# Optimization experiments

Hardware: AMD Instinct MI355X
Metric: run time of the kernel (lower is better)

The kernel has to match this reference:

```python
import jax, jax.numpy as jnp
import numpy as np

BETA = 0.25
N_EMBED = 1024
DIM = 256


def setup_inputs() -> dict:
    key = jax.random.key(0)
    k1, k2 = jax.random.split(key)
    z = jax.random.normal(k1, (8, DIM, 64, 64), dtype=jnp.float32)
    # matches nn.Embedding init: uniform(-1/n_embed, 1/n_embed)
    codebook = jax.random.uniform(
        k2, (N_EMBED, DIM), dtype=jnp.float32,
        minval=-1.0 / N_EMBED, maxval=1.0 / N_EMBED)
    return {"z": z, "codebook": codebook}


def reference(z, codebook):
    B, C, H, W = z.shape
    sg = jax.lax.stop_gradient
    zp = jnp.transpose(z, (0, 2, 3, 1))          # [B,H,W,C]
    zf = zp.reshape(-1, C)                        # [N,C], N = B*H*W
    # squared euclidean distances: ||z||^2 + ||e||^2 - 2 z.e
    d = (jnp.sum(zf * zf, axis=1, keepdims=True)
         + jnp.sum(codebook * codebook, axis=1)
         - 2.0 * zf @ codebook.T)                 # [N, n_embed]
    idx = jnp.argmin(d, axis=1)                   # [N]
    # one-hot @ codebook in the original is just an index gather
    z_q = codebook[idx].reshape(zp.shape)         # [B,H,W,C]
    loss = (BETA * jnp.mean((sg(z_q) - zp) ** 2)
            + jnp.mean((z_q - sg(zp)) ** 2))
    z_q_st = zp + sg(z_q - zp)                    # straight-through estimator
    z_q_out = jnp.transpose(z_q_st, (0, 3, 1, 2))  # back to NCHW
    return z_q_out, loss, idx.reshape(B, H, W)
```

## Files before the change

kernel.cpp:

```cpp
#include <hip/hip_runtime.h>
#include <hip/hip_fp16.h>

#define NELEM 8388608
#define M_GAP 6e-4f
#define SCORE_SCALE (-1.0f / 512.0f)

typedef _Float16 f16x8 __attribute__((ext_vector_type(8)));
typedef short s16x8 __attribute__((ext_vector_type(8)));
typedef float f32x4 __attribute__((ext_vector_type(4)));

__device__ __forceinline__ unsigned short bf16r(float f) {
  unsigned u = __float_as_uint(f);
  return (unsigned short)((u + 0x7fffu + ((u >> 16) & 1u)) >> 16);
}
__device__ __forceinline__ float bf16f(unsigned short h) {
  return __uint_as_float(((unsigned)h) << 16);
}

__device__ __forceinline__ float pw128_sq(const float* p, int s) {
  float r[8];
#pragma unroll
  for (int j = 0; j < 8; ++j) { float v = p[j * s]; r[j] = __fmul_rn(v, v); }
#pragma unroll
  for (int i = 8; i < 128; i += 8) {
#pragma unroll
    for (int j = 0; j < 8; ++j) {
      float v = p[(i + j) * s];
      r[j] = __fadd_rn(r[j], __fmul_rn(v, v));
    }
  }
  return __fadd_rn(__fadd_rn(__fadd_rn(r[0], r[1]), __fadd_rn(r[2], r[3])),
                   __fadd_rn(__fadd_rn(r[4], r[5]), __fadd_rn(r[6], r[7])));
}
__device__ __forceinline__ float np_sumsq256(const float* p, int s) {
  return __fadd_rn(pw128_sq(p, s), pw128_sq(p + 128 * s, s));
}

__global__ __launch_bounds__(256)
void vq_prep(const float* __restrict__ cb, unsigned short* __restrict__ cbimg,
             float* __restrict__ cbT, float* __restrict__ Bsg,
             unsigned* __restrict__ cnt, float* __restrict__ loss) {
  int gid = blockIdx.x * 256 + threadIdx.x;
  if (gid == 0) { *cnt = 0u; *loss = 0.0f; }
  int j = gid >> 2, qt = gid & 3;
  const float4* row4 = reinterpret_cast<const float4*>(cb + (size_t)j * 256 + qt * 64);
  int T = j >> 4, jj = j & 15;
  unsigned short* baseh = cbimg + (size_t)T * 4096 + jj * 256;
  int sw = jj << 3;
#pragma unroll
  for (int m = 0; m < 8; ++m) {
    int c0 = qt * 64 + m * 8;
    float4 va = row4[m * 2];
    float4 vb = row4[m * 2 + 1];
    float v[8] = {va.x, va.y, va.z, va.w, vb.x, vb.y, vb.z, vb.w};
    s16x8 hv;
#pragma unroll
    for (int q = 0; q < 8; ++q) {
      hv[q] = (short)__half_as_ushort(__float2half(v[q] * 1024.0f));
      cbT[(size_t)(c0 + q) * 1024 + j] = v[q];
    }
    *reinterpret_cast<s16x8*>(baseh + (c0 ^ sw)) = hv;
  }
  if (qt == 0) Bsg[j] = np_sumsq256(cb + (size_t)j * 256, 1);
}

__global__ __launch_bounds__(256, 2)
void vq_fast(const float* __restrict__ z, const float* __restrict__ cb,
             const unsigned short* __restrict__ cbimg,
             const float* __restrict__ Bsg,
             float* __restrict__ zq, float* __restrict__ loss,
             float* __restrict__ idxo,
             unsigned* __restrict__ list, unsigned* __restrict__ cnt,
             float* __restrict__ zdump) {
  __shared__ __align__(16) unsigned char buf[34816];
  __shared__ float BsL[1024];
  __shared__ float part[32][36];
  __shared__ float rowA[64];
  __shared__ int bestj[64];
  __shared__ float bestd[64];
  __shared__ unsigned char flg[64];
  __shared__ float wred[4];
  __shared__ float cv1[4 * 64], cv2[4 * 64];
  __shared__ int ci1[4 * 64];

  const int t = threadIdx.x;
  const int bid = blockIdx.x;
  const int lane = t & 63;
  const int wv = t >> 6;
  const int l15 = lane & 15;
  const int lk = lane >> 4;

  float* zt = reinterpret_cast<float*>(buf);
  const float4* z4 = reinterpret_cast<const float4*>(
      z + (size_t)(bid >> 6) * 1048576 + (size_t)(bid & 63) * 64);

  f16x8 ah[4][8];
  for (int hp = 0; hp < 2; ++hp) {
    float sq[4] = {0.f, 0.f, 0.f, 0.f};
#pragma unroll
    for (int i = 0; i < 8; ++i) {
      int idx = t + i * 256;
      int c = idx >> 3, w4p = idx & 7;
      float4 v = z4[(size_t)c * 1024 + hp * 8 + w4p];
      zt[c * 33 + w4p * 4 + 0] = v.x;
      zt[c * 33 + w4p * 4 + 1] = v.y;
      zt[c * 33 + w4p * 4 + 2] = v.z;
      zt[c * 33 + w4p * 4 + 3] = v.w;
      sq[0] += v.x * v.x; sq[1] += v.y * v.y;
      sq[2] += v.z * v.z; sq[3] += v.w * v.w;
    }
#pragma unroll
    for (int q = 0; q < 4; ++q) part[t >> 3][(t & 7) * 4 + q] = sq[q];
    __syncthreads();
    if (t < 32) {
      float s = 0.f;
#pragma unroll
      for (int g = 0; g < 32; ++g) s += part[g][t];
      rowA[hp * 32 + t] = s;
    }
#pragma unroll
    for (int rr2 = 0; rr2 < 2; ++rr2) {
      int rs = hp * 2 + rr2;
      int lr = rr2 * 16 + l15;
#pragma unroll
      for (int kk = 0; kk < 8; ++kk)
#pragma unroll
        for (int m = 0; m < 8; ++m)
          ah[rs][kk][m] = (_Float16)zt[(kk * 32 + lk * 8 + m) * 33 + lr];
    }
    if (zdump) {
#pragma unroll
      for (int i = 0; i < 8; ++i) {
        int item = t + i * 256;
        int c4 = item & 63, rowp = item >> 6;
        float4 v = make_float4(zt[(c4 * 4 + 0) * 33 + rowp],
                               zt[(c4 * 4 + 1) * 33 + rowp],
                               zt[(c4 * 4 + 2) * 33 + rowp],
                               zt[(c4 * 4 + 3) * 33 + rowp]);
        *reinterpret_cast<float4*>(
            zdump + ((size_t)bid * 64 + hp * 32 + rowp) * 256 + c4 * 4) = v;
      }
    }
    __syncthreads();
  }

  s16x8* sbuf = reinterpret_cast<s16x8*>(buf);
  const s16x8* cimg = reinterpret_cast<const s16x8*>(cbimg);
#pragma unroll
  for (int i = 0; i < 8; ++i) {
    int gidx = t + i * 256;
    sbuf[gidx] = cimg[(size_t)((gidx >> 9) * 16 + 0) * 512 + (gidx & 511)];
  }
  for (int i = t; i < 1024; i += 256) BsL[i] = Bsg[i];
  __syncthreads();

  float b1v[4][4], b2v[4][4];
  int b1i[4][4];
#pragma unroll
  for (int rs = 0; rs < 4; ++rs)
#pragma unroll
    for (int r = 0; r < 4; ++r) { b1v[rs][r] = 3.4e38f; b2v[rs][r] = 3.4e38f; b1i[rs][r] = 0; }

  const unsigned short* wbuf = reinterpret_cast<const unsigned short*>(buf) + wv * 4096;

  for (int it = 0; it < 16; ++it) {
    s16x8 g[8];
    if (it < 15) {
#pragma unroll
      for (int i = 0; i < 8; ++i) {
        int gidx = t + i * 256;
        g[i] = cimg[(size_t)((gidx >> 9) * 16 + it + 1) * 512 + (gidx & 511)];
      }
    }

    f32x4 acc[4];
#pragma unroll
    for (int rs = 0; rs < 4; ++rs) acc[rs] = (f32x4){0.f, 0.f, 0.f, 0.f};
#pragma unroll
    for (int kk = 0; kk < 8; ++kk) {
      int e = l15 * 256 + ((kk * 32 + lk * 8) ^ (l15 << 3));
      f16x8 bh = *reinterpret_cast<const f16x8*>(wbuf + e);
#pragma unroll
      for (int rs = 0; rs < 4; ++rs)
        acc[rs] = __builtin_amdgcn_mfma_f32_16x16x32_f16(ah[rs][kk], bh, acc[rs], 0, 0, 0);
    }

    {
      int j = wv * 256 + it * 16 + l15;
      float Bj = BsL[j];
#pragma unroll
      for (int rs = 0; rs < 4; ++rs)
#pragma unroll
        for (int r = 0; r < 4; ++r) {
          float s = fmaf(SCORE_SCALE, acc[rs][r], Bj);
          bool lt = s < b1v[rs][r];
          float other = lt ? b1v[rs][r] : s;
          b2v[rs][r] = fminf(b2v[rs][r], other);
          b1v[rs][r] = fminf(b1v[rs][r], s);
          b1i[rs][r] = lt ? j : b1i[rs][r];
        }
    }
    __syncthreads();
    if (it < 15) {
#pragma unroll
      for (int i = 0; i < 8; ++i) sbuf[t + i * 256] = g[i];
    }
    __syncthreads();
  }

#pragma unroll
  for (int mk = 1; mk < 16; mk <<= 1) {
#pragma unroll
    for (int rs = 0; rs < 4; ++rs)
#pragma unroll
      for (int r = 0; r < 4; ++r) {
        float ov1 = __shfl_xor(b1v[rs][r], mk, 64);
        float ov2 = __shfl_xor(b2v[rs][r], mk, 64);
        int oi1 = __shfl_xor(b1i[rs][r], mk, 64);
        bool lt = ov1 < b1v[rs][r];
        float hi = lt ? b1v[rs][r] : ov1;
        b2v[rs][r] = fminf(fminf(b2v[rs][r], ov2), hi);
        b1v[rs][r] = fminf(b1v[rs][r], ov1);
        b1i[rs][r] = lt ? oi1 : b1i[rs][r];
      }
  }
  if (l15 == 0) {
#pragma unroll
    for (int rs = 0; rs < 4; ++rs)
#pragma unroll
      for (int r = 0; r < 4; ++r) {
        int rr = rs * 16 + lk * 4 + r;
        cv1[wv * 64 + rr] = b1v[rs][r];
        cv2[wv * 64 + rr] = b2v[rs][r];
        ci1[wv * 64 + rr] = b1i[rs][r];
      }
  }
  __syncthreads();

  if (t < 64) {
    float v1 = cv1[t], v2 = cv2[t];
    int i1 = ci1[t];
#pragma unroll
    for (int w = 1; w < 4; ++w) {
      float u1 = cv1[w * 64 + t], u2 = cv2[w * 64 + t];
      int ui = ci1[w * 64 + t];
      if (u1 < v1) { v2 = fminf(v1, u2); v1 = u1; i1 = ui; }
      else v2 = fminf(v2, u1);
    }
    bestj[t] = i1;
    bestd[t] = v1;
    flg[t] = (v2 - v1 <= M_GAP) ? 1 : 0;
    int n = bid * 64 + t;
    idxo[n] = (float)i1;
    if (flg[t]) { unsigned pos = atomicAdd(cnt, 1u); list[pos] = (unsigned)n; }
  }
  __syncthreads();

  {
    float lv = (t < 64) ? (rowA[t] + bestd[t]) : 0.f;
#pragma unroll
    for (int off = 32; off > 0; off >>= 1) lv += __shfl_down(lv, off, 64);
    if (lane == 0) wred[wv] = lv;
  }
  __syncthreads();
  if (t == 0)
    atomicAdd(loss, (wred[0] + wred[1] + wred[2] + wred[3]) * (1.25f / (float)NELEM));

  f32x4* ldsF4 = reinterpret_cast<f32x4*>(buf);
  const float* ldsF = reinterpret_cast<const float*>(buf);
  const float4* cb4 = reinterpret_cast<const float4*>(cb);
  float* zqb = zq + (size_t)(bid >> 6) * 1048576 + (size_t)(bid & 63) * 64;
  for (int hp = 0; hp < 2; ++hp) {
    __syncthreads();
#pragma unroll
    for (int i = 0; i < 8; ++i) {
      int item = t + i * 256;
      int rr = item >> 6, cc = item & 63;
      float4 v = cb4[(size_t)bestj[hp * 32 + rr] * 64 + cc];
      ldsF4[rr * 64 + (cc ^ ((rr >> 2) & 7))] = (f32x4){v.x, v.y, v.z, v.w};
    }
    __syncthreads();
#pragma unroll
    for (int i = 0; i < 8; ++i) {
      int item = t + i * 256;
      int w4p = item & 7, c = item >> 3;
      float ov[4];
#pragma unroll
      for (int q = 0; q < 4; ++q) {
        int rr = w4p * 4 + q;
        ov[q] = ldsF[(rr * 64 + ((c >> 2) ^ ((rr >> 2) & 7))) * 4 + (c & 3)];
      }
      *reinterpret_cast<float4*>(zqb + (size_t)c * 4096 + hp * 32 + w4p * 4) =
          make_float4(ov[0], ov[1], ov[2], ov[3]);
    }
  }
}

__global__ __launch_bounds__(256)
void vq_exact_fast(const float* __restrict__ zdump, const float* __restrict__ cbT,
                   const float* __restrict__ Bsg, const unsigned* __restrict__ list,
                   const unsigned* __restrict__ cnt, float* __restrict__ idxo) {
  __shared__ float zr[8][260];
  __shared__ float Anp[8];
  __shared__ float rv[256];
  __shared__ int ri[256];
  const int t = threadIdx.x;
  const unsigned K = *cnt;
  const float4* cbT4 = reinterpret_cast<const float4*>(cbT);
  const float4* zd4 = reinterpret_cast<const float4*>(zdump);

  for (unsigned g = blockIdx.x; g * 8 < K; g += gridDim.x) {
    int nrows = (int)min(8u, K - g * 8);
    __syncthreads();
#pragma unroll
    for (int i = 0; i < 2; ++i) {
      int idx = t + i * 256;
      int r = idx >> 6, c4 = idx & 63;
      if (r < nrows) {
        float4 v = zd4[(size_t)list[g * 8 + r] * 64 + c4];
        zr[r][c4 * 4 + 0] = v.x; zr[r][c4 * 4 + 1] = v.y;
        zr[r][c4 * 4 + 2] = v.z; zr[r][c4 * 4 + 3] = v.w;
      }
    }
    __syncthreads();
    if (t < nrows) Anp[t] = np_sumsq256(&zr[t][0], 1);
    __syncthreads();

    float acc[8][4];
#pragma unroll
    for (int r = 0; r < 8; ++r)
#pragma unroll
      for (int q = 0; q < 4; ++q) acc[r][q] = 0.f;
    for (int c = 0; c < 256; ++c) {
      float4 bv = cbT4[c * 256 + t];
#pragma unroll
      for (int r = 0; r < 8; ++r) {
        float zc = zr[r][c];
        acc[r][0] = fmaf(zc, bv.x, acc[r][0]);
        acc[r][1] = fmaf(zc, bv.y, acc[r][1]);
        acc[r][2] = fmaf(zc, bv.z, acc[r][2]);
        acc[r][3] = fmaf(zc, bv.w, acc[r][3]);
      }
    }
    for (int r = 0; r < nrows; ++r) {
      float A = Anp[r];
      float bvv = 3.4e38f;
      int bii = 0;
#pragma unroll
      for (int q = 0; q < 4; ++q) {
        int j = t * 4 + q;
        float dd = __fsub_rn(__fadd_rn(A, Bsg[j]), __fmul_rn(2.0f, acc[r][q]));
        if (dd < bvv) { bvv = dd; bii = j; }
      }
      rv[t] = bvv; ri[t] = bii;
      __syncthreads();
      for (int s2 = 128; s2 > 0; s2 >>= 1) {
        if (t < s2) {
          float v2 = rv[t + s2]; int i2 = ri[t + s2];
          if (v2 < rv[t] || (v2 == rv[t] && i2 < ri[t])) { rv[t] = v2; ri[t] = i2; }
        }
        __syncthreads();
      }
      if (t == 0) idxo[list[g * 8 + r]] = (float)ri[0];
      __syncthreads();
    }
  }
}

__global__ __launch_bounds__(256)
void vq_exact_scatter(const float* __restrict__ z, const float* __restrict__ cbT,
                      const float* __restrict__ Bsg, const unsigned* __restrict__ list,
                      const unsigned* __restrict__ cnt, float* __restrict__ idxo) {
  __shared__ float zr[8][260];
  __shared__ float Anp[8];
  __shared__ float rv[256];
  __shared__ int ri[256];
  const int t = threadIdx.x;
  const unsigned K = *cnt;
  const float4* cbT4 = reinterpret_cast<const float4*>(cbT);

  for (unsigned g = blockIdx.x; g * 8 < K; g += gridDim.x) {
    int nrows = (int)min(8u, K - g * 8);
    __syncthreads();
    {
      int r = t >> 5, l32 = t & 31;
      if (r < nrows) {
        int n = (int)list[g * 8 + r];
        int b = n >> 12, hw = n & 4095;
        const float* zb = z + (size_t)b * 1048576 + hw;
#pragma unroll
        for (int q = 0; q < 8; ++q) {
          int c = l32 * 8 + q;
          zr[r][c] = zb[(size_t)c * 4096];
        }
      }
    }
    __syncthreads();
    if (t < nrows) Anp[t] = np_sumsq256(&zr[t][0], 1);
    __syncthreads();
    float acc[8][4];
#pragma unroll
    for (int r = 0; r < 8; ++r)
#pragma unroll
      for (int q = 0; q < 4; ++q) acc[r][q] = 0.f;
    for (int c = 0; c < 256; ++c) {
      float4 bv = cbT4[c * 256 + t];
#pragma unroll
      for (int r = 0; r < 8; ++r) {
        float zc = zr[r][c];
        acc[r][0] = fmaf(zc, bv.x, acc[r][0]);
        acc[r][1] = fmaf(zc, bv.y, acc[r][1]);
        acc[r][2] = fmaf(zc, bv.z, acc[r][2]);
        acc[r][3] = fmaf(zc, bv.w, acc[r][3]);
      }
    }
    for (int r = 0; r < nrows; ++r) {
      float A = Anp[r];
      float bvv = 3.4e38f;
      int bii = 0;
#pragma unroll
      for (int q = 0; q < 4; ++q) {
        int j = t * 4 + q;
        float dd = __fsub_rn(__fadd_rn(A, Bsg[j]), __fmul_rn(2.0f, acc[r][q]));
        if (dd < bvv) { bvv = dd; bii = j; }
      }
      rv[t] = bvv; ri[t] = bii;
      __syncthreads();
      for (int s2 = 128; s2 > 0; s2 >>= 1) {
        if (t < s2) {
          float v2 = rv[t + s2]; int i2 = ri[t + s2];
          if (v2 < rv[t] || (v2 == rv[t] && i2 < ri[t])) { rv[t] = v2; ri[t] = i2; }
        }
        __syncthreads();
      }
      if (t == 0) idxo[list[g * 8 + r]] = (float)ri[0];
      __syncthreads();
    }
  }
}

__global__ __launch_bounds__(256)
void vq_ref(const float* __restrict__ z, const float* __restrict__ cb,
            float* __restrict__ zq, float* __restrict__ loss,
            float* __restrict__ idxo) {
  __shared__ __align__(16) float zt[256 * 64];
  __shared__ __align__(16) float cbt[256 * 64];
  __shared__ float As[64];
  __shared__ float Bs[64];
  __shared__ int bestj[64];
  __shared__ float cand_v[16 * 64];
  __shared__ int cand_i[16 * 64];
  __shared__ double wred[4];
  const int t = threadIdx.x;
  const int wg = t & 15, jg = t >> 4;
  const int bid = blockIdx.x;
  const int b = bid >> 6, h = bid & 63;
  const int n0 = bid * 64;
  const float4* z4 = reinterpret_cast<const float4*>(z + (size_t)b * 256 * 4096 + (size_t)h * 64);
  float4* zt4 = reinterpret_cast<float4*>(zt);
#pragma unroll
  for (int i = 0; i < 16; ++i) {
    int idx4 = t + i * 256;
    zt4[idx4] = z4[(size_t)(idx4 >> 4) * 1024 + (idx4 & 15)];
  }
  __syncthreads();
  if (t < 64) As[t] = np_sumsq256(zt + t, 64);
  float bv[4]; int bi[4];
#pragma unroll
  for (int a = 0; a < 4; ++a) { bv[a] = 3.4e38f; bi[a] = 0; }
  for (int p = 0; p < 16; ++p) {
    __syncthreads();
    const float4* cb4 = reinterpret_cast<const float4*>(cb) + (size_t)p * 64 * 64;
#pragma unroll
    for (int i = 0; i < 16; ++i) {
      int idx4 = t + i * 256;
      int jj = idx4 >> 6, c4 = idx4 & 63;
      float4 v = cb4[idx4];
      cbt[(c4 * 4 + 0) * 64 + jj] = v.x;
      cbt[(c4 * 4 + 1) * 64 + jj] = v.y;
      cbt[(c4 * 4 + 2) * 64 + jj] = v.z;
      cbt[(c4 * 4 + 3) * 64 + jj] = v.w;
    }
    __syncthreads();
    if (t < 64) Bs[t] = np_sumsq256(cbt + t, 64);
    float acc[4][4];
#pragma unroll
    for (int a = 0; a < 4; ++a)
#pragma unroll
      for (int u = 0; u < 4; ++u) acc[a][u] = 0.0f;
    const float4* ztp = reinterpret_cast<const float4*>(zt) + wg;
    const float4* cbp = reinterpret_cast<const float4*>(cbt) + jg;
#pragma unroll 4
    for (int c = 0; c < 256; ++c) {
      float4 zv = ztp[c * 16];
      float4 cv = cbp[c * 16];
      float za[4] = {zv.x, zv.y, zv.z, zv.w};
      float ca[4] = {cv.x, cv.y, cv.z, cv.w};
#pragma unroll
      for (int a = 0; a < 4; ++a)
#pragma unroll
        for (int u = 0; u < 4; ++u) acc[a][u] = fmaf(za[a], ca[u], acc[a][u]);
    }
    __syncthreads();
#pragma unroll
    for (int u = 0; u < 4; ++u) {
      int j = p * 64 + jg * 4 + u;
      float Bju = Bs[jg * 4 + u];
#pragma unroll
      for (int a = 0; a < 4; ++a) {
        float AB = __fadd_rn(As[wg * 4 + a], Bju);
        float dd = __fsub_rn(AB, __fmul_rn(2.0f, acc[a][u]));
        if (dd < bv[a]) { bv[a] = dd; bi[a] = j; }
      }
    }
  }
  __syncthreads();
#pragma unroll
  for (int a = 0; a < 4; ++a) {
    int w = wg * 4 + a;
    cand_v[jg * 64 + w] = bv[a];
    cand_i[jg * 64 + w] = bi[a];
  }
  __syncthreads();
  if (t < 64) {
    float v0 = cand_v[t]; int i0 = cand_i[t];
    for (int g = 1; g < 16; ++g) {
      float v = cand_v[g * 64 + t]; int ii = cand_i[g * 64 + t];
      if (v < v0 || (v == v0 && ii < i0)) { v0 = v; i0 = ii; }
    }
    bestj[t] = i0;
    idxo[n0 + t] = (float)i0;
  }
  __syncthreads();
  double lsum = 0.0;
  float* zqbase = zq + (size_t)b * 256 * 4096 + (size_t)h * 64;
  for (int i = 0; i < 64; ++i) {
    int idx = t + i * 256;
    int c = idx >> 6, w = idx & 63;
    float zvv = zt[c * 64 + w];
    float cvv = cb[(size_t)bestj[w] * 256 + c];
    zqbase[(size_t)c * 4096 + w] = cvv;
    double d = (double)cvv - (double)zvv;
    lsum += d * d;
  }
#pragma unroll
  for (int off = 32; off > 0; off >>= 1) lsum += __shfl_down(lsum, off, 64);
  if ((t & 63) == 0) wred[t >> 6] = lsum;
  __syncthreads();
  if (t == 0) {
    double tot = wred[0] + wred[1] + wred[2] + wred[3];
    atomicAdd(loss, (float)(tot * (1.25 / (double)NELEM)));
  }
}

extern "C" void kernel_launch(void* const* d_in, const int* in_sizes, int n_in,
                              void* d_out, int out_size, void* d_ws, size_t ws_size,
                              hipStream_t stream) {
  (void)in_sizes; (void)n_in; (void)out_size;
  const float* z = (const float*)d_in[0];
  const float* cb = (const float*)d_in[1];
  float* out = (float*)d_out;
  float* zq = out;
  float* loss = out + NELEM;
  float* idxo = out + NELEM + 1;
  if (ws_size < 1712128) {
    hipMemsetAsync(loss, 0, sizeof(float), stream);
    vq_ref<<<512, 256, 0, stream>>>(z, cb, zq, loss, idxo);
    return;
  }
  unsigned char* ws = (unsigned char*)d_ws;
  unsigned* cnt = (unsigned*)ws;
  float* Bsg = (float*)(ws + 1024);
  unsigned* list = (unsigned*)(ws + 8192);
  float* cbT = (float*)(ws + 139264);
  unsigned short* cbimg = (unsigned short*)(ws + 1187840);
  const bool have_dump = (ws_size >= 35651584);
  float* zdump = have_dump ? (float*)(ws + 2097152) : nullptr;
  vq_prep<<<16, 256, 0, stream>>>(cb, cbimg, cbT, Bsg, cnt, loss);
  vq_fast<<<512, 256, 0, stream>>>(z, cb, cbimg, Bsg, zq, loss, idxo, list, cnt, zdump);
  if (have_dump)
    vq_exact_fast<<<512, 256, 0, stream>>>(zdump, cbT, Bsg, list, cnt, idxo);
  else
    vq_exact_scatter<<<512, 256, 0, stream>>>(z, cbT, Bsg, list, cnt, idxo);
}
```

Measured before the change: 103.6 us.

## Load codebook MFMA fragments directly from global into registers, dropping LDS staging

The prep kernel now writes the fp16 codebook image in an MFMA-fragment-ordered layout, so each lane can load its B operand with one coalesced 16-byte global read per k-step. The main loop double-buffers these fragments in registers (ba/bb) instead of staging tiles through shared memory, which removes the two block-wide barriers per iteration and the LDS writes and reads. It also starts the first codebook fragment and norm loads before the z transpose. In exchange it uses 64 more VGPRs per thread under a 2-blocks-per-CU launch bound, and every wave now reads its codebook slice from L2 on its own instead of sharing one block-level copy.

```diff
diff --git a/kernel.cpp b/kernel.cpp
--- a/kernel.cpp
+++ b/kernel.cpp
@@ -45,13 +45,12 @@
   int j = gid >> 2, qt = gid & 3;
   const float4* row4 = reinterpret_cast<const float4*>(cb + (size_t)j * 256 + qt * 64);
   int T = j >> 4, jj = j & 15;
-  unsigned short* baseh = cbimg + (size_t)T * 4096 + jj * 256;
-  int sw = jj << 3;
-#pragma unroll
-  for (int m = 0; m < 8; ++m) {
-    int c0 = qt * 64 + m * 8;
-    float4 va = row4[m * 2];
-    float4 vb = row4[m * 2 + 1];
+#pragma unroll
+  for (int m8 = 0; m8 < 8; ++m8) {
+    int c0 = qt * 64 + m8 * 8;
+    int kk = c0 >> 5, lk = (c0 >> 3) & 3;
+    float4 va = row4[m8 * 2];
+    float4 vb = row4[m8 * 2 + 1];
     float v[8] = {va.x, va.y, va.z, va.w, vb.x, vb.y, vb.z, vb.w};
     s16x8 hv;
 #pragma unroll
@@ -59,7 +58,7 @@
       hv[q] = (short)__half_as_ushort(__float2half(v[q] * 1024.0f));
       cbT[(size_t)(c0 + q) * 1024 + j] = v[q];
     }
-    *reinterpret_cast<s16x8*>(baseh + (c0 ^ sw)) = hv;
+    *reinterpret_cast<s16x8*>(cbimg + (size_t)T * 4096 + kk * 512 + (lk * 16 + jj) * 8) = hv;
   }
   if (qt == 0) Bsg[j] = np_sumsq256(cb + (size_t)j * 256, 1);
 }
@@ -90,9 +89,17 @@
   const int l15 = lane & 15;
   const int lk = lane >> 4;
 
+  const f16x8* cimg2 = reinterpret_cast<const f16x8*>(cbimg);
   float* zt = reinterpret_cast<float*>(buf);
   const float4* z4 = reinterpret_cast<const float4*>(
       z + (size_t)(bid >> 6) * 1048576 + (size_t)(bid & 63) * 64);
+
+  f16x8 ba[8], bb[8];
+#pragma unroll
+  for (int kk = 0; kk < 8; ++kk)
+    ba[kk] = cimg2[(size_t)(wv * 16) * 512 + kk * 64 + lane];
+
+  for (int i = t; i < 1024; i += 256) BsL[i] = Bsg[i];
 
   f16x8 ah[4][8];
   for (int hp = 0; hp < 2; ++hp) {
@@ -144,16 +151,6 @@
     __syncthreads();
   }
 
-  s16x8* sbuf = reinterpret_cast<s16x8*>(buf);
-  const s16x8* cimg = reinterpret_cast<const s16x8*>(cbimg);
-#pragma unroll
-  for (int i = 0; i < 8; ++i) {
-    int gidx = t + i * 256;
-    sbuf[gidx] = cimg[(size_t)((gidx >> 9) * 16 + 0) * 512 + (gidx & 511)];
-  }
-  for (int i = t; i < 1024; i += 256) BsL[i] = Bsg[i];
-  __syncthreads();
-
   float b1v[4][4], b2v[4][4];
   int b1i[4][4];
 #pragma unroll
@@ -161,51 +158,41 @@
 #pragma unroll
     for (int r = 0; r < 4; ++r) { b1v[rs][r] = 3.4e38f; b2v[rs][r] = 3.4e38f; b1i[rs][r] = 0; }
 
-  const unsigned short* wbuf = reinterpret_cast<const unsigned short*>(buf) + wv * 4096;
-
-  for (int it = 0; it < 16; ++it) {
-    s16x8 g[8];
-    if (it < 15) {
-#pragma unroll
-      for (int i = 0; i < 8; ++i) {
-        int gidx = t + i * 256;
-        g[i] = cimg[(size_t)((gidx >> 9) * 16 + it + 1) * 512 + (gidx & 511)];
-      }
-    }
-
+  auto step = [&](const f16x8* bfr, int it2) {
     f32x4 acc[4];
 #pragma unroll
     for (int rs = 0; rs < 4; ++rs) acc[rs] = (f32x4){0.f, 0.f, 0.f, 0.f};
 #pragma unroll
-    for (int kk = 0; kk < 8; ++kk) {
-      int e = l15 * 256 + ((kk * 32 + lk * 8) ^ (l15 << 3));
-      f16x8 bh = *reinterpret_cast<const f16x8*>(wbuf + e);
+    for (int kk = 0; kk < 8; ++kk)
 #pragma unroll
       for (int rs = 0; rs < 4; ++rs)
-        acc[rs] = __builtin_amdgcn_mfma_f32_16x16x32_f16(ah[rs][kk], bh, acc[rs], 0, 0, 0);
-    }
-
-    {
-      int j = wv * 256 + it * 16 + l15;
-      float Bj = BsL[j];
-#pragma unroll
-      for (int rs = 0; rs < 4; ++rs)
-#pragma unroll
-        for (int r = 0; r < 4; ++r) {
-          float s = fmaf(SCORE_SCALE, acc[rs][r], Bj);
-          bool lt = s < b1v[rs][r];
-          float other = lt ? b1v[rs][r] : s;
-          b2v[rs][r] = fminf(b2v[rs][r], other);
-          b1v[rs][r] = fminf(b1v[rs][r], s);
-          b1i[rs][r] = lt ? j : b1i[rs][r];
-        }
-    }
-    __syncthreads();
-    if (it < 15) {
-#pragma unroll
-      for (int i = 0; i < 8; ++i) sbuf[t + i * 256] = g[i];
-    }
-    __syncthreads();
+        acc[rs] = __builtin_amdgcn_mfma_f32_16x16x32_f16(ah[rs][kk], bfr[kk], acc[rs], 0, 0, 0);
+    int j = wv * 256 + it2 * 16 + l15;
+    float Bj = BsL[j];
+#pragma unroll
+    for (int rs = 0; rs < 4; ++rs)
+#pragma unroll
+      for (int r = 0; r < 4; ++r) {
+        float s = fmaf(SCORE_SCALE, acc[rs][r], Bj);
+        bool lt = s < b1v[rs][r];
+        float other = lt ? b1v[rs][r] : s;
+        b2v[rs][r] = fminf(b2v[rs][r], other);
+        b1v[rs][r] = fminf(b1v[rs][r], s);
+        b1i[rs][r] = lt ? j : b1i[rs][r];
+      }
+  };
+
+  for (int it = 0; it < 16; it += 2) {
+#pragma unroll
+    for (int kk = 0; kk < 8; ++kk)
+      bb[kk] = cimg2[(size_t)(wv * 16 + it + 1) * 512 + kk * 64 + lane];
+    step(ba, it);
+    if (it + 2 < 16) {
+#pragma unroll
+      for (int kk = 0; kk < 8; ++kk)
+        ba[kk] = cimg2[(size_t)(wv * 16 + it + 2) * 512 + kk * 64 + lane];
+    }
+    step(bb, it + 1);
   }
 
 #pragma unroll
```

Result: slower. 125.1 us (+20.7%).
